# Kernel tuning notes

Measured on AMD Instinct MI355X. Metric: run time of the kernel, lower is better.

Reference implementation:

```python
import jax, jax.numpy as jnp
import numpy as np

INPUT_DIM = 128
OUTPUT_DIM = 256
BATCH = 4096

def setup_inputs() -> dict:
    key = jax.random.key(0)
    k_x, k_w1, k_b1, k_w2, k_b2 = jax.random.split(key, 5)
    d = INPUT_DIM
    h = 2 * OUTPUT_DIM
    x = jax.random.normal(k_x, (BATCH, d), dtype=jnp.float32)
    # Linear weights stored as [in, out]; scale ~ torch default init
    W1 = jax.random.uniform(k_w1, (d * d, h), dtype=jnp.float32, minval=-1, maxval=1) / np.sqrt(d * d)
    b1 = jax.random.uniform(k_b1, (h,), dtype=jnp.float32, minval=-1, maxval=1) / np.sqrt(d * d)
    W2 = jax.random.uniform(k_w2, (h, OUTPUT_DIM), dtype=jnp.float32, minval=-1, maxval=1) / np.sqrt(h)
    b2 = jax.random.uniform(k_b2, (OUTPUT_DIM,), dtype=jnp.float32, minval=-1, maxval=1) / np.sqrt(h)
    return {"x": x, "W1": W1, "b1": b1, "W2": W2, "b2": b2}

def reference(x, W1, b1, W2, b2):
    B, d = x.shape
    # torch bmm of the two expanded copies: tp[b,i,j] = sum_k x[b,i]*x[b,j] = d * x[b,i]*x[b,j]
    tp = jnp.asarray(d, x.dtype) * jnp.einsum('bi,bj->bij', x, x)  # [B, d, d]
    flat = tp.reshape(B, d * d)
    h = jax.nn.relu(flat @ W1 + b1)  # [B, 2*output_dim]
    return h @ W2 + b2               # [B, output_dim]
```

## Files before the change

kernel.cpp:

```cpp
#include <hip/hip_runtime.h>
#include <hip/hip_bf16.h>


typedef __attribute__((ext_vector_type(8))) short short8;
typedef __attribute__((ext_vector_type(4))) float floatx4;

__device__ __forceinline__ unsigned short f2bf(float f) {
    union { float f; unsigned int u; } v; v.f = f;
    unsigned int r = v.u + 0x7fffu + ((v.u >> 16) & 1u);
    return (unsigned short)(r >> 16);
}
__device__ __forceinline__ float bf2f(unsigned short b) {
    union { unsigned int u; float f; } v; v.u = ((unsigned int)b) << 16;
    return v.f;
}

__global__ __launch_bounds__(256) void pack_w1_kernel(
    const float* __restrict__ W1, unsigned short* __restrict__ W1Tp) {
    __shared__ float tile[64][65];
    const int k0 = blockIdx.x * 64;
    const int c0 = blockIdx.y * 64;
    const int tr = threadIdx.x >> 4;
    const int tc4 = (threadIdx.x & 15) * 4;
#pragma unroll
    for (int p = 0; p < 4; ++p) {
        int k = p * 16 + tr;
        float4 v = *(const float4*)(W1 + (long)(k0 + k) * 512 + c0 + tc4);
        tile[k][tc4 + 0] = v.x; tile[k][tc4 + 1] = v.y;
        tile[k][tc4 + 2] = v.z; tile[k][tc4 + 3] = v.w;
    }
    __syncthreads();
    const int lane = threadIdx.x & 63;
    const int w = threadIdx.x >> 6;
    const int m = lane & 15, quad = lane >> 4;
#pragma unroll
    for (int pass = 0; pass < 2; ++pass) {
        int chunk = w * 2 + pass;
        int kcL = chunk & 1, c16L = chunk >> 1;
        union { unsigned short s[8]; uint4 u; } o;
#pragma unroll
        for (int j = 0; j < 8; ++j)
            o.s[j] = f2bf(tile[kcL * 32 + quad * 8 + j][c16L * 16 + m]);
        long c16g = (c0 >> 4) + c16L;
        long kcg  = (k0 >> 5) + kcL;
        *(uint4*)(W1Tp + (c16g * 512 + kcg) * 512 + lane * 8) = o.u;
    }
}

__global__ __launch_bounds__(256) void transpose_cast_kernel(
    const float* __restrict__ in, unsigned short* __restrict__ out, int R, int C) {
    __shared__ float tile[64][65];
    const int r0 = blockIdx.x * 64, c0 = blockIdx.y * 64;
    const int tr = threadIdx.x >> 4;
    const int tc4 = (threadIdx.x & 15) * 4;
#pragma unroll
    for (int p = 0; p < 4; ++p) {
        int r = p * 16 + tr;
        float4 v = *(const float4*)(in + (long)(r0 + r) * C + c0 + tc4);
        tile[r][tc4 + 0] = v.x; tile[r][tc4 + 1] = v.y;
        tile[r][tc4 + 2] = v.z; tile[r][tc4 + 3] = v.w;
    }
    __syncthreads();
#pragma unroll
    for (int p = 0; p < 4; ++p) {
        int c = p * 16 + tr;
        union { unsigned short s[4]; uint2 u; } pk;
#pragma unroll
        for (int e = 0; e < 4; ++e) pk.s[e] = f2bf(tile[tc4 + e][c]);
        *(uint2*)(out + (long)(c0 + c) * R + r0 + tc4) = pk.u;
    }
}

__global__ __launch_bounds__(256, 2) void gemm1_kernel(
    const float* __restrict__ x,
    const unsigned short* __restrict__ W1Tp,
    unsigned short* __restrict__ Pb) {
    __shared__ float xT[256][34];
    const int tid = threadIdx.x;
    const int b0 = blockIdx.x * 256;
    const int c0 = blockIdx.y * 64;
    const int zi = blockIdx.z;
    const int i0 = zi * 32;

    for (int idx = tid; idx < 256 * 32; idx += 256) {
        int bL = idx >> 5, iL = idx & 31;
        xT[bL][iL] = x[(long)(b0 + bL) * 128 + i0 + iL];
    }
    __syncthreads();

    const int wid = tid >> 6;
    const int wm = wid >> 1, wn = wid & 1;
    const int lane = tid & 63;
    const int n16 = lane & 15, quad = lane >> 4;
    const int bBase = b0 + wn * 128;
    const int c16base = (c0 >> 4) + wm * 2;
    const int bLloc = wn * 128 + n16;

    floatx4 acc[2][8];
#pragma unroll
    for (int tm = 0; tm < 2; ++tm)
#pragma unroll
        for (int tn = 0; tn < 8; ++tn) acc[tm][tn] = (floatx4){0.f, 0.f, 0.f, 0.f};
    const floatx4 zero4 = (floatx4){0.f, 0.f, 0.f, 0.f};

#pragma unroll
    for (int jh = 0; jh < 2; ++jh) {
        short8 Xf[2][8];
#pragma unroll
        for (int ks = 0; ks < 2; ++ks)
#pragma unroll
            for (int tn = 0; tn < 8; ++tn) {
                const float* xp = x + (long)(bBase + tn * 16 + n16) * 128
                                    + jh * 64 + ks * 32 + quad * 8;
                float4 v0 = *(const float4*)xp;
                float4 v1 = *(const float4*)(xp + 4);
                short8 f;
                f[0] = (short)f2bf(v0.x); f[1] = (short)f2bf(v0.y);
                f[2] = (short)f2bf(v0.z); f[3] = (short)f2bf(v0.w);
                f[4] = (short)f2bf(v1.x); f[5] = (short)f2bf(v1.y);
                f[6] = (short)f2bf(v1.z); f[7] = (short)f2bf(v1.w);
                Xf[ks][tn] = f;
            }
        const unsigned short* aBase[2][2];
#pragma unroll
        for (int tm = 0; tm < 2; ++tm)
#pragma unroll
            for (int ks = 0; ks < 2; ++ks)
                aBase[tm][ks] = W1Tp
                    + ((long)(c16base + tm) * 512 + (long)i0 * 4 + jh * 2 + ks) * 512
                    + lane * 8;

        short8 Abuf[2][2][2];
#pragma unroll
        for (int tm = 0; tm < 2; ++tm)
#pragma unroll
            for (int ks = 0; ks < 2; ++ks) {
                Abuf[0][tm][ks] = *(const short8*)(aBase[tm][ks]);
                Abuf[1][tm][ks] = *(const short8*)(aBase[tm][ks] + 2048);
            }

#pragma unroll 2
        for (int i = 0; i < 32; ++i) {
            const int st = i & 1;
            float xi[8];
#pragma unroll
            for (int tn = 0; tn < 8; ++tn)
                xi[tn] = xT[bLloc + tn * 16][i];
#pragma unroll
            for (int tm = 0; tm < 2; ++tm)
#pragma unroll
                for (int tn = 0; tn < 8; ++tn) {
                    floatx4 t = __builtin_amdgcn_mfma_f32_16x16x32_bf16(
                        Abuf[st][tm][0], Xf[0][tn], zero4, 0, 0, 0);
                    t = __builtin_amdgcn_mfma_f32_16x16x32_bf16(
                        Abuf[st][tm][1], Xf[1][tn], t, 0, 0, 0);
                    acc[tm][tn] += xi[tn] * t;
                }
            const int pi = (i + 2) & 31;
#pragma unroll
            for (int tm = 0; tm < 2; ++tm)
#pragma unroll
                for (int ks = 0; ks < 2; ++ks)
                    Abuf[st][tm][ks] =
                        *(const short8*)(aBase[tm][ks] + (long)pi * 2048);
        }
    }

    unsigned short* pb = Pb + (long)zi * (4096L * 512);
#pragma unroll
    for (int tm = 0; tm < 2; ++tm)
#pragma unroll
        for (int tn = 0; tn < 8; ++tn) {
            int b = bBase + tn * 16 + n16;
            int cb = (c16base + tm) * 16 + quad * 4;
            union { unsigned short s[4]; uint2 u; } pk;
#pragma unroll
            for (int r = 0; r < 4; ++r) pk.s[r] = f2bf(acc[tm][tn][r]);
            *(uint2*)(pb + (long)b * 512 + cb) = pk.u;
        }
}

__global__ __launch_bounds__(256) void tail_kernel(
    const unsigned short* __restrict__ Pb,
    const float* __restrict__ b1,
    const unsigned short* __restrict__ W2T,
    const float* __restrict__ b2,
    float* __restrict__ out) {
    __shared__ unsigned short hL[16][516];
    __shared__ float b1s[512];
    const int tid = threadIdx.x;
    const int b0 = blockIdx.x * 16;
    b1s[tid] = b1[tid];
    b1s[tid + 256] = b1[tid + 256];
    __syncthreads();

    const unsigned int* Pu = (const unsigned int*)Pb;
#pragma unroll 4
    for (int idx = tid; idx < 16 * 256; idx += 256) {
        int bL = idx >> 8;
        int cu = idx & 255;
        float s0 = 0.f, s1 = 0.f;
#pragma unroll
        for (int z = 0; z < 4; ++z) {
            unsigned int u = Pu[((long)z * 4096 + b0 + bL) * 256 + cu];
            s0 += bf2f((unsigned short)(u & 0xffff));
            s1 += bf2f((unsigned short)(u >> 16));
        }
        int c = cu * 2;
        float v0 = fmaxf(fmaf(128.f, s0, b1s[c]), 0.f);
        float v1 = fmaxf(fmaf(128.f, s1, b1s[c + 1]), 0.f);
        unsigned int pk = (unsigned int)f2bf(v0) | ((unsigned int)f2bf(v1) << 16);
        *(unsigned int*)&hL[bL][c] = pk;
    }
    __syncthreads();

    const int w = tid >> 6, lane = tid & 63;
    const int n16 = lane & 15, quad = lane >> 4;
    const int o0 = w * 64;
    floatx4 acc[4];
#pragma unroll
    for (int tn = 0; tn < 4; ++tn) acc[tn] = (floatx4){0.f, 0.f, 0.f, 0.f};

#pragma unroll 4
    for (int ks = 0; ks < 16; ++ks) {
        short8 Af, Bf[4];
        {
            const unsigned short* p = &hL[n16][ks * 32 + quad * 8];
            union { uint2 u[2]; short8 s; } cvt;
            cvt.u[0] = *(const uint2*)p;
            cvt.u[1] = *(const uint2*)(p + 4);
            Af = cvt.s;
        }
#pragma unroll
        for (int tn = 0; tn < 4; ++tn)
            Bf[tn] = *(const short8*)(W2T + (long)(o0 + tn * 16 + n16) * 512
                                      + ks * 32 + quad * 8);
#pragma unroll
        for (int tn = 0; tn < 4; ++tn)
            acc[tn] = __builtin_amdgcn_mfma_f32_16x16x32_bf16(
                Af, Bf[tn], acc[tn], 0, 0, 0);
    }
#pragma unroll
    for (int tn = 0; tn < 4; ++tn) {
        float bias = b2[o0 + tn * 16 + n16];
#pragma unroll
        for (int r = 0; r < 4; ++r)
            out[(long)(b0 + quad * 4 + r) * 256
                + o0 + tn * 16 + n16] = acc[tn][r] + bias;
    }
}

extern "C" void kernel_launch(void* const* d_in, const int* in_sizes, int n_in,
                              void* d_out, int out_size, void* d_ws, size_t ws_size,
                              hipStream_t stream) {
    const float* x  = (const float*)d_in[0];
    const float* W1 = (const float*)d_in[1];
    const float* b1 = (const float*)d_in[2];
    const float* W2 = (const float*)d_in[3];
    const float* b2 = (const float*)d_in[4];
    float* out = (float*)d_out;

    char* ws = (char*)d_ws;
    unsigned short* W1Tp = (unsigned short*)(ws);
    unsigned short* W2T  = (unsigned short*)(ws + 16777216);
    unsigned short* Pb   = (unsigned short*)(ws + 16777216 + 262144);

    pack_w1_kernel<<<dim3(256, 8), 256, 0, stream>>>(W1, W1Tp);
    transpose_cast_kernel<<<dim3(8, 4), 256, 0, stream>>>(W2, W2T, 512, 256);
    gemm1_kernel<<<dim3(16, 8, 4), 256, 0, stream>>>(x, W1Tp, Pb);
    tail_kernel<<<dim3(256), 256, 0, stream>>>(Pb, b1, W2T, b2, out);
}
```

Baseline: 175.0 us.

## Shrink gemm1 block tile to 128 batch rows and one column tile per warp

Each gemm1 block now covers 128 batch rows instead of 256, and each warp owns a single 16-column strip of W1 instead of two. The grid doubles in x, which halves accumulator registers and shared memory per block and should allow more concurrent waves and better CU fill. The A-fragment double buffering is rewritten as an explicit two-stage manually unrolled loop with named registers in place of an indexed array. In exchange, each W1 fragment is reused across fewer batch rows, so global/L2 traffic for W1 roughly doubles.

New measurement: 184.7 us. +5.6%, slower.

```diff
diff --git a/kernel.cpp b/kernel.cpp
--- a/kernel.cpp
+++ b/kernel.cpp
@@ -75,32 +75,27 @@
     const float* __restrict__ x,
     const unsigned short* __restrict__ W1Tp,
     unsigned short* __restrict__ Pb) {
-    __shared__ float xT[256][34];
+    __shared__ float xT[128][33];
     const int tid = threadIdx.x;
-    const int b0 = blockIdx.x * 256;
+    const int b0 = blockIdx.x * 128;
     const int c0 = blockIdx.y * 64;
     const int zi = blockIdx.z;
     const int i0 = zi * 32;
 
-    for (int idx = tid; idx < 256 * 32; idx += 256) {
+    for (int idx = tid; idx < 128 * 32; idx += 256) {
         int bL = idx >> 5, iL = idx & 31;
         xT[bL][iL] = x[(long)(b0 + bL) * 128 + i0 + iL];
     }
     __syncthreads();
 
     const int wid = tid >> 6;
-    const int wm = wid >> 1, wn = wid & 1;
     const int lane = tid & 63;
     const int n16 = lane & 15, quad = lane >> 4;
-    const int bBase = b0 + wn * 128;
-    const int c16base = (c0 >> 4) + wm * 2;
-    const int bLloc = wn * 128 + n16;
-
-    floatx4 acc[2][8];
-#pragma unroll
-    for (int tm = 0; tm < 2; ++tm)
-#pragma unroll
-        for (int tn = 0; tn < 8; ++tn) acc[tm][tn] = (floatx4){0.f, 0.f, 0.f, 0.f};
+    const int c16 = (c0 >> 4) + wid;
+
+    floatx4 acc[8];
+#pragma unroll
+    for (int tn = 0; tn < 8; ++tn) acc[tn] = (floatx4){0.f, 0.f, 0.f, 0.f};
     const floatx4 zero4 = (floatx4){0.f, 0.f, 0.f, 0.f};
 
 #pragma unroll
@@ -110,7 +105,7 @@
         for (int ks = 0; ks < 2; ++ks)
 #pragma unroll
             for (int tn = 0; tn < 8; ++tn) {
-                const float* xp = x + (long)(bBase + tn * 16 + n16) * 128
+                const float* xp = x + (long)(b0 + tn * 16 + n16) * 128
                                     + jh * 64 + ks * 32 + quad * 8;
                 float4 v0 = *(const float4*)xp;
                 float4 v1 = *(const float4*)(xp + 4);
@@ -121,63 +116,65 @@
                 f[6] = (short)f2bf(v1.z); f[7] = (short)f2bf(v1.w);
                 Xf[ks][tn] = f;
             }
-        const unsigned short* aBase[2][2];
-#pragma unroll
-        for (int tm = 0; tm < 2; ++tm)
-#pragma unroll
-            for (int ks = 0; ks < 2; ++ks)
-                aBase[tm][ks] = W1Tp
-                    + ((long)(c16base + tm) * 512 + (long)i0 * 4 + jh * 2 + ks) * 512
-                    + lane * 8;
-
-        short8 Abuf[2][2][2];
-#pragma unroll
-        for (int tm = 0; tm < 2; ++tm)
-#pragma unroll
-            for (int ks = 0; ks < 2; ++ks) {
-                Abuf[0][tm][ks] = *(const short8*)(aBase[tm][ks]);
-                Abuf[1][tm][ks] = *(const short8*)(aBase[tm][ks] + 2048);
-            }
-
-#pragma unroll 2
-        for (int i = 0; i < 32; ++i) {
-            const int st = i & 1;
-            float xi[8];
-#pragma unroll
-            for (int tn = 0; tn < 8; ++tn)
-                xi[tn] = xT[bLloc + tn * 16][i];
-#pragma unroll
-            for (int tm = 0; tm < 2; ++tm)
+        const unsigned short* aB0 = W1Tp
+            + ((long)c16 * 512 + (long)i0 * 4 + jh * 2) * 512 + lane * 8;
+        const unsigned short* aB1 = aB0 + 512;
+
+        short8 A00 = *(const short8*)(aB0);
+        short8 A01 = *(const short8*)(aB1);
+        short8 A10 = *(const short8*)(aB0 + 2048);
+        short8 A11 = *(const short8*)(aB1 + 2048);
+
+#pragma unroll 1
+        for (int ib = 0; ib < 16; ++ib) {
+            const int i = ib * 2;
+            {
+                float xi[8];
+#pragma unroll
+                for (int tn = 0; tn < 8; ++tn)
+                    xi[tn] = xT[n16 + tn * 16][i];
 #pragma unroll
                 for (int tn = 0; tn < 8; ++tn) {
                     floatx4 t = __builtin_amdgcn_mfma_f32_16x16x32_bf16(
-                        Abuf[st][tm][0], Xf[0][tn], zero4, 0, 0, 0);
+                        A00, Xf[0][tn], zero4, 0, 0, 0);
                     t = __builtin_amdgcn_mfma_f32_16x16x32_bf16(
-                        Abuf[st][tm][1], Xf[1][tn], t, 0, 0, 0);
-                    acc[tm][tn] += xi[tn] * t;
+                        A01, Xf[1][tn], t, 0, 0, 0);
+                    acc[tn] += xi[tn] * t;
                 }
-            const int pi = (i + 2) & 31;
-#pragma unroll
-            for (int tm = 0; tm < 2; ++tm)
-#pragma unroll
-                for (int ks = 0; ks < 2; ++ks)
-                    Abuf[st][tm][ks] =
-                        *(const short8*)(aBase[tm][ks] + (long)pi * 2048);
+                const int p = (i + 2) & 31;
+                A00 = *(const short8*)(aB0 + (long)p * 2048);
+                A01 = *(const short8*)(aB1 + (long)p * 2048);
+            }
+            {
+                float xi[8];
+#pragma unroll
+                for (int tn = 0; tn < 8; ++tn)
+                    xi[tn] = xT[n16 + tn * 16][i + 1];
+#pragma unroll
+                for (int tn = 0; tn < 8; ++tn) {
+                    floatx4 t = __builtin_amdgcn_mfma_f32_16x16x32_bf16(
+                        A10, Xf[0][tn], zero4, 0, 0, 0);
+                    t = __builtin_amdgcn_mfma_f32_16x16x32_bf16(
+                        A11, Xf[1][tn], t, 0, 0, 0);
+                    acc[tn] += xi[tn] * t;
+                }
+                const int p = (i + 3) & 31;
+                A10 = *(const short8*)(aB0 + (long)p * 2048);
+                A11 = *(const short8*)(aB1 + (long)p * 2048);
+            }
         }
     }
 
     unsigned short* pb = Pb + (long)zi * (4096L * 512);
 #pragma unroll
-    for (int tm = 0; tm < 2; ++tm)
-#pragma unroll
-        for (int tn = 0; tn < 8; ++tn) {
-            int b = bBase + tn * 16 + n16;
-            int cb = (c16base + tm) * 16 + quad * 4;
-            union { unsigned short s[4]; uint2 u; } pk;
-#pragma unroll
-            for (int r = 0; r < 4; ++r) pk.s[r] = f2bf(acc[tm][tn][r]);
-            *(uint2*)(pb + (long)b * 512 + cb) = pk.u;
-        }
+    for (int tn = 0; tn < 8; ++tn) {
+        int b = b0 + tn * 16 + n16;
+        int cb = c16 * 16 + quad * 4;
+        union { unsigned short s[4]; uint2 u; } pk;
+#pragma unroll
+        for (int r = 0; r < 4; ++r) pk.s[r] = f2bf(acc[tn][r]);
+        *(uint2*)(pb + (long)b * 512 + cb) = pk.u;
+    }
 }
 
 __global__ __launch_bounds__(256) void tail_kernel(
@@ -267,6 +264,6 @@
 
     pack_w1_kernel<<<dim3(256, 8), 256, 0, stream>>>(W1, W1Tp);
     transpose_cast_kernel<<<dim3(8, 4), 256, 0, stream>>>(W2, W2T, 512, 256);
-    gemm1_kernel<<<dim3(16, 8, 4), 256, 0, stream>>>(x, W1Tp, Pb);
+    gemm1_kernel<<<dim3(32, 8, 4), 256, 0, stream>>>(x, W1Tp, Pb);
     tail_kernel<<<dim3(256), 256, 0, stream>>>(Pb, b1, W2T, b2, out);
 }
```

## Deepen W1 register prefetch to four stages and swizzle gemm1 block order

Applied to the files above, without the earlier changes.

The inner loop of gemm1 now keeps four stages of W1 fragments in named registers instead of a two-stage array, prefetching four iterations ahead through a macro-unrolled step. This is meant to hide global-load latency behind more MFMA work and to avoid dynamic array indexing. The 3D grid is flattened to 1D and remapped so that consecutive blocks are spread across different batch, column and z tiles, which changes how blocks are distributed over XCDs and how cache locality falls out. Extra prefetch registers can raise register pressure under the two-blocks-per-CU launch bound.

New measurement: 175.7 us. No clear change (+0.4%).

```diff
diff --git a/kernel.cpp b/kernel.cpp
--- a/kernel.cpp
+++ b/kernel.cpp
@@ -71,15 +71,44 @@
     }
 }
 
+
+#define A_STEP(Ac00, Ac01, Ac10, Ac11, I)                                  \
+    {                                                                      \
+        float xi[8];                                                       \
+        _Pragma("unroll")                                                  \
+        for (int tn = 0; tn < 8; ++tn)                                     \
+            xi[tn] = xT[bLloc + tn * 16][(I)];                             \
+        _Pragma("unroll")                                                  \
+        for (int tn = 0; tn < 8; ++tn) {                                   \
+            floatx4 t0 = __builtin_amdgcn_mfma_f32_16x16x32_bf16(          \
+                Ac00, Xf[0][tn], zero4, 0, 0, 0);                          \
+            t0 = __builtin_amdgcn_mfma_f32_16x16x32_bf16(                  \
+                Ac01, Xf[1][tn], t0, 0, 0, 0);                             \
+            acc[0][tn] += xi[tn] * t0;                                     \
+            floatx4 t1 = __builtin_amdgcn_mfma_f32_16x16x32_bf16(          \
+                Ac10, Xf[0][tn], zero4, 0, 0, 0);                          \
+            t1 = __builtin_amdgcn_mfma_f32_16x16x32_bf16(                  \
+                Ac11, Xf[1][tn], t1, 0, 0, 0);                             \
+            acc[1][tn] += xi[tn] * t1;                                     \
+        }                                                                  \
+        const int p_ = ((I) + 4) & 31;     \
+        Ac00 = *(const short8*)(aB00 + (long)p_ * 2048);                   \
+        Ac01 = *(const short8*)(aB01 + (long)p_ * 2048);                   \
+        Ac10 = *(const short8*)(aB10 + (long)p_ * 2048);                   \
+        Ac11 = *(const short8*)(aB11 + (long)p_ * 2048);                   \
+    }
+
 __global__ __launch_bounds__(256, 2) void gemm1_kernel(
     const float* __restrict__ x,
     const unsigned short* __restrict__ W1Tp,
     unsigned short* __restrict__ Pb) {
     __shared__ float xT[256][34];
     const int tid = threadIdx.x;
-    const int b0 = blockIdx.x * 256;
-    const int c0 = blockIdx.y * 64;
-    const int zi = blockIdx.z;
+    const int n = blockIdx.x;
+    const int L = (n & 7) * 64 + (n >> 3);
+    const int b0 = (L & 15) * 256;
+    const int c0 = ((L >> 4) & 7) * 64;
+    const int zi = L >> 7;
     const int i0 = zi * 32;
 
     for (int idx = tid; idx < 256 * 32; idx += 256) {
@@ -121,48 +150,39 @@
                 f[6] = (short)f2bf(v1.z); f[7] = (short)f2bf(v1.w);
                 Xf[ks][tn] = f;
             }
-        const unsigned short* aBase[2][2];
-#pragma unroll
-        for (int tm = 0; tm < 2; ++tm)
-#pragma unroll
-            for (int ks = 0; ks < 2; ++ks)
-                aBase[tm][ks] = W1Tp
-                    + ((long)(c16base + tm) * 512 + (long)i0 * 4 + jh * 2 + ks) * 512
-                    + lane * 8;
-
-        short8 Abuf[2][2][2];
-#pragma unroll
-        for (int tm = 0; tm < 2; ++tm)
-#pragma unroll
-            for (int ks = 0; ks < 2; ++ks) {
-                Abuf[0][tm][ks] = *(const short8*)(aBase[tm][ks]);
-                Abuf[1][tm][ks] = *(const short8*)(aBase[tm][ks] + 2048);
-            }
-
-#pragma unroll 2
-        for (int i = 0; i < 32; ++i) {
-            const int st = i & 1;
-            float xi[8];
-#pragma unroll
-            for (int tn = 0; tn < 8; ++tn)
-                xi[tn] = xT[bLloc + tn * 16][i];
-#pragma unroll
-            for (int tm = 0; tm < 2; ++tm)
-#pragma unroll
-                for (int tn = 0; tn < 8; ++tn) {
-                    floatx4 t = __builtin_amdgcn_mfma_f32_16x16x32_bf16(
-                        Abuf[st][tm][0], Xf[0][tn], zero4, 0, 0, 0);
-                    t = __builtin_amdgcn_mfma_f32_16x16x32_bf16(
-                        Abuf[st][tm][1], Xf[1][tn], t, 0, 0, 0);
-                    acc[tm][tn] += xi[tn] * t;
-                }
-            const int pi = (i + 2) & 31;
-#pragma unroll
-            for (int tm = 0; tm < 2; ++tm)
-#pragma unroll
-                for (int ks = 0; ks < 2; ++ks)
-                    Abuf[st][tm][ks] =
-                        *(const short8*)(aBase[tm][ks] + (long)pi * 2048);
+        const unsigned short* aB00 = W1Tp
+            + ((long)(c16base + 0) * 512 + (long)i0 * 4 + jh * 2 + 0) * 512
+            + lane * 8;
+        const unsigned short* aB01 = aB00 + 512;
+        const unsigned short* aB10 = W1Tp
+            + ((long)(c16base + 1) * 512 + (long)i0 * 4 + jh * 2 + 0) * 512
+            + lane * 8;
+        const unsigned short* aB11 = aB10 + 512;
+
+        short8 A0_00 = *(const short8*)(aB00);
+        short8 A0_01 = *(const short8*)(aB01);
+        short8 A0_10 = *(const short8*)(aB10);
+        short8 A0_11 = *(const short8*)(aB11);
+        short8 A1_00 = *(const short8*)(aB00 + 1 * 2048);
+        short8 A1_01 = *(const short8*)(aB01 + 1 * 2048);
+        short8 A1_10 = *(const short8*)(aB10 + 1 * 2048);
+        short8 A1_11 = *(const short8*)(aB11 + 1 * 2048);
+        short8 A2_00 = *(const short8*)(aB00 + 2 * 2048);
+        short8 A2_01 = *(const short8*)(aB01 + 2 * 2048);
+        short8 A2_10 = *(const short8*)(aB10 + 2 * 2048);
+        short8 A2_11 = *(const short8*)(aB11 + 2 * 2048);
+        short8 A3_00 = *(const short8*)(aB00 + 3 * 2048);
+        short8 A3_01 = *(const short8*)(aB01 + 3 * 2048);
+        short8 A3_10 = *(const short8*)(aB10 + 3 * 2048);
+        short8 A3_11 = *(const short8*)(aB11 + 3 * 2048);
+
+#pragma unroll 1
+        for (int ib = 0; ib < 8; ++ib) {
+            const int i = ib * 4;
+            A_STEP(A0_00, A0_01, A0_10, A0_11, i + 0)
+            A_STEP(A1_00, A1_01, A1_10, A1_11, i + 1)
+            A_STEP(A2_00, A2_01, A2_10, A2_11, i + 2)
+            A_STEP(A3_00, A3_01, A3_10, A3_11, i + 3)
         }
     }
 
@@ -267,6 +287,6 @@
 
     pack_w1_kernel<<<dim3(256, 8), 256, 0, stream>>>(W1, W1Tp);
     transpose_cast_kernel<<<dim3(8, 4), 256, 0, stream>>>(W2, W2T, 512, 256);
-    gemm1_kernel<<<dim3(16, 8, 4), 256, 0, stream>>>(x, W1Tp, Pb);
+    gemm1_kernel<<<dim3(512), 256, 0, stream>>>(x, W1Tp, Pb);
     tail_kernel<<<dim3(256), 256, 0, stream>>>(Pb, b1, W2T, b2, out);
 }
```

## Exploit outer-product symmetry to fold W1 into upper-triangular packed weights

Applied to the files above, without the earlier changes.

Because x_i*x_j is symmetric, the prep kernel folds W1[i,j]+W1[j,i] into an upper-triangular packed bf16 weight, so the first GEMM reads about 10 of 16 K-blocks. The first GEMM now covers the full K range per block instead of splitting over four z partitions. This removes the bf16 partial-sum buffer and the reduction pass, and bias plus ReLU move into the GEMM epilogue. The two prep kernels are merged into one launch, and the block-index mappings are swizzled. Folding the weight pairs before rounding to bf16 changes rounding slightly, and each GEMM block now has fewer output tiles and loops over more K.

After: 186.2 us. +6.4%, slower.

```diff
diff --git a/kernel.cpp b/kernel.cpp
--- a/kernel.cpp
+++ b/kernel.cpp
@@ -10,81 +10,130 @@
     unsigned int r = v.u + 0x7fffu + ((v.u >> 16) & 1u);
     return (unsigned short)(r >> 16);
 }
-__device__ __forceinline__ float bf2f(unsigned short b) {
-    union { unsigned int u; float f; } v; v.u = ((unsigned int)b) << 16;
-    return v.f;
-}
-
-__global__ __launch_bounds__(256) void pack_w1_kernel(
-    const float* __restrict__ W1, unsigned short* __restrict__ W1Tp) {
+
+__global__ __launch_bounds__(256) void prep_kernel(
+    const float* __restrict__ W1, unsigned short* __restrict__ W1p,
+    const float* __restrict__ W2, unsigned short* __restrict__ W2T) {
     __shared__ float tile[64][65];
-    const int k0 = blockIdx.x * 64;
-    const int c0 = blockIdx.y * 64;
-    const int tr = threadIdx.x >> 4;
-    const int tc4 = (threadIdx.x & 15) * 4;
-#pragma unroll
-    for (int p = 0; p < 4; ++p) {
-        int k = p * 16 + tr;
-        float4 v = *(const float4*)(W1 + (long)(k0 + k) * 512 + c0 + tc4);
-        tile[k][tc4 + 0] = v.x; tile[k][tc4 + 1] = v.y;
-        tile[k][tc4 + 2] = v.z; tile[k][tc4 + 3] = v.w;
-    }
-    __syncthreads();
-    const int lane = threadIdx.x & 63;
-    const int w = threadIdx.x >> 6;
-    const int m = lane & 15, quad = lane >> 4;
-#pragma unroll
-    for (int pass = 0; pass < 2; ++pass) {
-        int chunk = w * 2 + pass;
-        int kcL = chunk & 1, c16L = chunk >> 1;
-        union { unsigned short s[8]; uint4 u; } o;
-#pragma unroll
-        for (int j = 0; j < 8; ++j)
-            o.s[j] = f2bf(tile[kcL * 32 + quad * 8 + j][c16L * 16 + m]);
-        long c16g = (c0 >> 4) + c16L;
-        long kcg  = (k0 >> 5) + kcL;
-        *(uint4*)(W1Tp + (c16g * 512 + kcg) * 512 + lane * 8) = o.u;
-    }
-}
-
-__global__ __launch_bounds__(256) void transpose_cast_kernel(
-    const float* __restrict__ in, unsigned short* __restrict__ out, int R, int C) {
-    __shared__ float tile[64][65];
-    const int r0 = blockIdx.x * 64, c0 = blockIdx.y * 64;
-    const int tr = threadIdx.x >> 4;
-    const int tc4 = (threadIdx.x & 15) * 4;
-#pragma unroll
-    for (int p = 0; p < 4; ++p) {
-        int r = p * 16 + tr;
-        float4 v = *(const float4*)(in + (long)(r0 + r) * C + c0 + tc4);
-        tile[r][tc4 + 0] = v.x; tile[r][tc4 + 1] = v.y;
-        tile[r][tc4 + 2] = v.z; tile[r][tc4 + 3] = v.w;
-    }
-    __syncthreads();
-#pragma unroll
-    for (int p = 0; p < 4; ++p) {
-        int c = p * 16 + tr;
-        union { unsigned short s[4]; uint2 u; } pk;
-#pragma unroll
-        for (int e = 0; e < 4; ++e) pk.s[e] = f2bf(tile[tc4 + e][c]);
-        *(uint2*)(out + (long)(c0 + c) * R + r0 + tc4) = pk.u;
-    }
-}
-
-__global__ __launch_bounds__(256, 2) void gemm1_kernel(
+    const int bx = blockIdx.x;
+    if (bx < 320) {
+        const int cb = bx & 7;
+        const int ih = (bx >> 3) & 3;
+        const int p  = bx >> 5;
+        int zi, zj;
+        if (p < 4)      { zi = 0; zj = p; }
+        else if (p < 7) { zi = 1; zj = p - 3; }
+        else if (p < 9) { zi = 2; zj = p - 5; }
+        else            { zi = 3; zj = 3; }
+        const int lane = threadIdx.x & 63;
+        const int w = threadIdx.x >> 6;
+        const int m = lane & 15, quad = lane >> 4;
+        const int c16 = cb * 4 + w;
+        const int c = c16 * 16 + m;
+        const int cum = (zi == 0) ? 0 : (zi == 1) ? 128 : (zi == 2) ? 224 : 288;
+        for (int il8 = 0; il8 < 8; ++il8) {
+            const int il = ih * 8 + il8;
+            const int i_g = zi * 32 + il;
+            union { unsigned short s[8]; uint4 u; } o;
+#pragma unroll
+            for (int e = 0; e < 8; ++e) {
+                const int j_g = zj * 32 + quad * 8 + e;
+                float v = 0.f;
+                if (j_g == i_g)
+                    v = W1[((long)i_g * 128 + j_g) * 512 + c];
+                else if (j_g > i_g)
+                    v = W1[((long)i_g * 128 + j_g) * 512 + c]
+                      + W1[((long)j_g * 128 + i_g) * 512 + c];
+                o.s[e] = f2bf(v);
+            }
+            const long chunk = (long)c16 * 320 + cum
+                             + (long)il * (4 - zi) + (zj - zi);
+            *(uint4*)(W1p + chunk * 512 + lane * 8) = o.u;
+        }
+    } else {
+        const int t = bx - 320;
+        const int r0 = (t & 7) * 64, c0 = (t >> 3) * 64;
+        const int R = 512, C = 256;
+        const int tr = threadIdx.x >> 4;
+        const int tc4 = (threadIdx.x & 15) * 4;
+#pragma unroll
+        for (int pp = 0; pp < 4; ++pp) {
+            int r = pp * 16 + tr;
+            float4 v = *(const float4*)(W2 + (long)(r0 + r) * C + c0 + tc4);
+            tile[r][tc4 + 0] = v.x; tile[r][tc4 + 1] = v.y;
+            tile[r][tc4 + 2] = v.z; tile[r][tc4 + 3] = v.w;
+        }
+        __syncthreads();
+#pragma unroll
+        for (int pp = 0; pp < 4; ++pp) {
+            int cc = pp * 16 + tr;
+            union { unsigned short s[4]; uint2 u; } pk;
+#pragma unroll
+            for (int e = 0; e < 4; ++e) pk.s[e] = f2bf(tile[tc4 + e][cc]);
+            *(uint2*)(W2T + (long)(c0 + cc) * R + r0 + tc4) = pk.u;
+        }
+    }
+}
+
+
+#define Z_PHASE(CH, ZB)                                                     \
+    {                                                                       \
+        short8 Ar[2][2][CH];                                                \
+        _Pragma("unroll")                                                   \
+        for (int q = 0; q < CH; ++q) {                                      \
+            Ar[0][0][q] = *(const short8*)(aP0 + (long)q * 512);            \
+            Ar[0][1][q] = *(const short8*)(aP1 + (long)q * 512);            \
+            Ar[1][0][q] = *(const short8*)(aP0 + (long)(CH + q) * 512);     \
+            Ar[1][1][q] = *(const short8*)(aP1 + (long)(CH + q) * 512);     \
+        }                                                                   \
+        _Pragma("unroll 2")                                                 \
+        for (int il = 0; il < 32; ++il) {                                   \
+            const int st = il & 1;                                          \
+            float xi0 = xT[xrow0][(ZB) * 32 + il];                          \
+            float xi1 = xT[xrow1][(ZB) * 32 + il];                          \
+            floatx4 t00 = zero4, t01 = zero4, t10 = zero4, t11 = zero4;     \
+            _Pragma("unroll")                                               \
+            for (int q = 0; q < CH; ++q) {                                  \
+                t00 = __builtin_amdgcn_mfma_f32_16x16x32_bf16(              \
+                    Ar[st][0][q], Xf[4 - (CH) + q][0], t00, 0, 0, 0);       \
+                t01 = __builtin_amdgcn_mfma_f32_16x16x32_bf16(              \
+                    Ar[st][0][q], Xf[4 - (CH) + q][1], t01, 0, 0, 0);       \
+                t10 = __builtin_amdgcn_mfma_f32_16x16x32_bf16(              \
+                    Ar[st][1][q], Xf[4 - (CH) + q][0], t10, 0, 0, 0);       \
+                t11 = __builtin_amdgcn_mfma_f32_16x16x32_bf16(              \
+                    Ar[st][1][q], Xf[4 - (CH) + q][1], t11, 0, 0, 0);       \
+            }                                                               \
+            acc[0][0] += xi0 * t00; acc[0][1] += xi1 * t01;                 \
+            acc[1][0] += xi0 * t10; acc[1][1] += xi1 * t11;                 \
+            _Pragma("unroll")                                               \
+            for (int q = 0; q < CH; ++q) {                                  \
+                Ar[st][0][q] = *(const short8*)(aP0                         \
+                    + (long)((il + 2) * (CH) + q) * 512);                   \
+                Ar[st][1][q] = *(const short8*)(aP1                         \
+                    + (long)((il + 2) * (CH) + q) * 512);                   \
+            }                                                               \
+        }                                                                   \
+        aP0 += 32 * (CH) * 512;                                             \
+        aP1 += 32 * (CH) * 512;                                             \
+    }
+
+__global__ __launch_bounds__(256, 2) void gemm_sym_kernel(
     const float* __restrict__ x,
-    const unsigned short* __restrict__ W1Tp,
-    unsigned short* __restrict__ Pb) {
-    __shared__ float xT[256][34];
+    const unsigned short* __restrict__ W1p,
+    const float* __restrict__ b1,
+    unsigned short* __restrict__ H) {
+    __shared__ float xT[64][129];
     const int tid = threadIdx.x;
-    const int b0 = blockIdx.x * 256;
-    const int c0 = blockIdx.y * 64;
-    const int zi = blockIdx.z;
-    const int i0 = zi * 32;
-
-    for (int idx = tid; idx < 256 * 32; idx += 256) {
-        int bL = idx >> 5, iL = idx & 31;
-        xT[bL][iL] = x[(long)(b0 + bL) * 128 + i0 + iL];
+    const int n = blockIdx.x;
+    const int L = (n & 7) * 64 + (n >> 3);
+    const int b0 = (L & 63) * 64;
+    const int c0 = (L >> 6) * 64;
+
+    for (int idx = tid; idx < 64 * 32; idx += 256) {
+        int bL = idx >> 5, i4 = (idx & 31) * 4;
+        float4 v = *(const float4*)(x + (long)(b0 + bL) * 128 + i4);
+        xT[bL][i4 + 0] = v.x; xT[bL][i4 + 1] = v.y;
+        xT[bL][i4 + 2] = v.z; xT[bL][i4 + 3] = v.w;
     }
     __syncthreads();
 
@@ -92,128 +141,70 @@
     const int wm = wid >> 1, wn = wid & 1;
     const int lane = tid & 63;
     const int n16 = lane & 15, quad = lane >> 4;
-    const int bBase = b0 + wn * 128;
+    const int bBase = b0 + wn * 32;
     const int c16base = (c0 >> 4) + wm * 2;
-    const int bLloc = wn * 128 + n16;
-
-    floatx4 acc[2][8];
+    const int xrow0 = wn * 32 + n16;
+    const int xrow1 = xrow0 + 16;
+
+    floatx4 acc[2][2];
 #pragma unroll
     for (int tm = 0; tm < 2; ++tm)
 #pragma unroll
-        for (int tn = 0; tn < 8; ++tn) acc[tm][tn] = (floatx4){0.f, 0.f, 0.f, 0.f};
+        for (int tn = 0; tn < 2; ++tn) acc[tm][tn] = (floatx4){0.f, 0.f, 0.f, 0.f};
     const floatx4 zero4 = (floatx4){0.f, 0.f, 0.f, 0.f};
 
-#pragma unroll
-    for (int jh = 0; jh < 2; ++jh) {
-        short8 Xf[2][8];
-#pragma unroll
-        for (int ks = 0; ks < 2; ++ks)
-#pragma unroll
-            for (int tn = 0; tn < 8; ++tn) {
-                const float* xp = x + (long)(bBase + tn * 16 + n16) * 128
-                                    + jh * 64 + ks * 32 + quad * 8;
-                float4 v0 = *(const float4*)xp;
-                float4 v1 = *(const float4*)(xp + 4);
-                short8 f;
-                f[0] = (short)f2bf(v0.x); f[1] = (short)f2bf(v0.y);
-                f[2] = (short)f2bf(v0.z); f[3] = (short)f2bf(v0.w);
-                f[4] = (short)f2bf(v1.x); f[5] = (short)f2bf(v1.y);
-                f[6] = (short)f2bf(v1.z); f[7] = (short)f2bf(v1.w);
-                Xf[ks][tn] = f;
-            }
-        const unsigned short* aBase[2][2];
-#pragma unroll
-        for (int tm = 0; tm < 2; ++tm)
-#pragma unroll
-            for (int ks = 0; ks < 2; ++ks)
-                aBase[tm][ks] = W1Tp
-                    + ((long)(c16base + tm) * 512 + (long)i0 * 4 + jh * 2 + ks) * 512
-                    + lane * 8;
-
-        short8 Abuf[2][2][2];
-#pragma unroll
-        for (int tm = 0; tm < 2; ++tm)
-#pragma unroll
-            for (int ks = 0; ks < 2; ++ks) {
-                Abuf[0][tm][ks] = *(const short8*)(aBase[tm][ks]);
-                Abuf[1][tm][ks] = *(const short8*)(aBase[tm][ks] + 2048);
-            }
-
-#pragma unroll 2
-        for (int i = 0; i < 32; ++i) {
-            const int st = i & 1;
-            float xi[8];
-#pragma unroll
-            for (int tn = 0; tn < 8; ++tn)
-                xi[tn] = xT[bLloc + tn * 16][i];
-#pragma unroll
-            for (int tm = 0; tm < 2; ++tm)
-#pragma unroll
-                for (int tn = 0; tn < 8; ++tn) {
-                    floatx4 t = __builtin_amdgcn_mfma_f32_16x16x32_bf16(
-                        Abuf[st][tm][0], Xf[0][tn], zero4, 0, 0, 0);
-                    t = __builtin_amdgcn_mfma_f32_16x16x32_bf16(
-                        Abuf[st][tm][1], Xf[1][tn], t, 0, 0, 0);
-                    acc[tm][tn] += xi[tn] * t;
-                }
-            const int pi = (i + 2) & 31;
-#pragma unroll
-            for (int tm = 0; tm < 2; ++tm)
-#pragma unroll
-                for (int ks = 0; ks < 2; ++ks)
-                    Abuf[st][tm][ks] =
-                        *(const short8*)(aBase[tm][ks] + (long)pi * 2048);
-        }
-    }
-
-    unsigned short* pb = Pb + (long)zi * (4096L * 512);
-#pragma unroll
-    for (int tm = 0; tm < 2; ++tm)
-#pragma unroll
-        for (int tn = 0; tn < 8; ++tn) {
+    short8 Xf[4][2];
+#pragma unroll
+    for (int kc = 0; kc < 4; ++kc)
+#pragma unroll
+        for (int tn = 0; tn < 2; ++tn) {
+            const float* xp = x + (long)(bBase + tn * 16 + n16) * 128
+                                + kc * 32 + quad * 8;
+            float4 v0 = *(const float4*)xp;
+            float4 v1 = *(const float4*)(xp + 4);
+            short8 f;
+            f[0] = (short)f2bf(v0.x); f[1] = (short)f2bf(v0.y);
+            f[2] = (short)f2bf(v0.z); f[3] = (short)f2bf(v0.w);
+            f[4] = (short)f2bf(v1.x); f[5] = (short)f2bf(v1.y);
+            f[6] = (short)f2bf(v1.z); f[7] = (short)f2bf(v1.w);
+            Xf[kc][tn] = f;
+        }
+
+    const unsigned short* aP0 = W1p + (long)(c16base + 0) * 320 * 512 + lane * 8;
+    const unsigned short* aP1 = W1p + (long)(c16base + 1) * 320 * 512 + lane * 8;
+
+    Z_PHASE(4, 0)
+    Z_PHASE(3, 1)
+    Z_PHASE(2, 2)
+    Z_PHASE(1, 3)
+
+#pragma unroll
+    for (int tm = 0; tm < 2; ++tm) {
+        const int cb4 = (c16base + tm) * 16 + quad * 4;
+        float4 b1v = *(const float4*)(b1 + cb4);
+#pragma unroll
+        for (int tn = 0; tn < 2; ++tn) {
             int b = bBase + tn * 16 + n16;
-            int cb = (c16base + tm) * 16 + quad * 4;
             union { unsigned short s[4]; uint2 u; } pk;
-#pragma unroll
-            for (int r = 0; r < 4; ++r) pk.s[r] = f2bf(acc[tm][tn][r]);
-            *(uint2*)(pb + (long)b * 512 + cb) = pk.u;
-        }
+            pk.s[0] = f2bf(fmaxf(fmaf(128.f, acc[tm][tn][0], b1v.x), 0.f));
+            pk.s[1] = f2bf(fmaxf(fmaf(128.f, acc[tm][tn][1], b1v.y), 0.f));
+            pk.s[2] = f2bf(fmaxf(fmaf(128.f, acc[tm][tn][2], b1v.z), 0.f));
+            pk.s[3] = f2bf(fmaxf(fmaf(128.f, acc[tm][tn][3], b1v.w), 0.f));
+            *(uint2*)(H + (long)b * 512 + cb4) = pk.u;
+        }
+    }
 }
 
 __global__ __launch_bounds__(256) void tail_kernel(
-    const unsigned short* __restrict__ Pb,
-    const float* __restrict__ b1,
+    const unsigned short* __restrict__ H,
     const unsigned short* __restrict__ W2T,
     const float* __restrict__ b2,
     float* __restrict__ out) {
-    __shared__ unsigned short hL[16][516];
-    __shared__ float b1s[512];
     const int tid = threadIdx.x;
-    const int b0 = blockIdx.x * 16;
-    b1s[tid] = b1[tid];
-    b1s[tid + 256] = b1[tid + 256];
-    __syncthreads();
-
-    const unsigned int* Pu = (const unsigned int*)Pb;
-#pragma unroll 4
-    for (int idx = tid; idx < 16 * 256; idx += 256) {
-        int bL = idx >> 8;
-        int cu = idx & 255;
-        float s0 = 0.f, s1 = 0.f;
-#pragma unroll
-        for (int z = 0; z < 4; ++z) {
-            unsigned int u = Pu[((long)z * 4096 + b0 + bL) * 256 + cu];
-            s0 += bf2f((unsigned short)(u & 0xffff));
-            s1 += bf2f((unsigned short)(u >> 16));
-        }
-        int c = cu * 2;
-        float v0 = fmaxf(fmaf(128.f, s0, b1s[c]), 0.f);
-        float v1 = fmaxf(fmaf(128.f, s1, b1s[c + 1]), 0.f);
-        unsigned int pk = (unsigned int)f2bf(v0) | ((unsigned int)f2bf(v1) << 16);
-        *(unsigned int*)&hL[bL][c] = pk;
-    }
-    __syncthreads();
-
+    const int n = blockIdx.x;
+    const int v = n >> 3;
+    const int bt = (n & 7) * 4 + (v & 3) + (v >> 2) * 32;
+    const int b0 = bt * 16;
     const int w = tid >> 6, lane = tid & 63;
     const int n16 = lane & 15, quad = lane >> 4;
     const int o0 = w * 64;
@@ -223,14 +214,9 @@
 
 #pragma unroll 4
     for (int ks = 0; ks < 16; ++ks) {
-        short8 Af, Bf[4];
-        {
-            const unsigned short* p = &hL[n16][ks * 32 + quad * 8];
-            union { uint2 u[2]; short8 s; } cvt;
-            cvt.u[0] = *(const uint2*)p;
-            cvt.u[1] = *(const uint2*)(p + 4);
-            Af = cvt.s;
-        }
+        short8 Af = *(const short8*)(H + (long)(b0 + n16) * 512
+                                     + ks * 32 + quad * 8);
+        short8 Bf[4];
 #pragma unroll
         for (int tn = 0; tn < 4; ++tn)
             Bf[tn] = *(const short8*)(W2T + (long)(o0 + tn * 16 + n16) * 512
@@ -261,12 +247,11 @@
     float* out = (float*)d_out;
 
     char* ws = (char*)d_ws;
-    unsigned short* W1Tp = (unsigned short*)(ws);
-    unsigned short* W2T  = (unsigned short*)(ws + 16777216);
-    unsigned short* Pb   = (unsigned short*)(ws + 16777216 + 262144);
-
-    pack_w1_kernel<<<dim3(256, 8), 256, 0, stream>>>(W1, W1Tp);
-    transpose_cast_kernel<<<dim3(8, 4), 256, 0, stream>>>(W2, W2T, 512, 256);
-    gemm1_kernel<<<dim3(16, 8, 4), 256, 0, stream>>>(x, W1Tp, Pb);
-    tail_kernel<<<dim3(256), 256, 0, stream>>>(Pb, b1, W2T, b2, out);
-}
+    unsigned short* W1p = (unsigned short*)(ws);
+    unsigned short* W2T = (unsigned short*)(ws + 10485760);
+    unsigned short* H   = (unsigned short*)(ws + 10485760 + 262144);
+
+    prep_kernel<<<dim3(352), 256, 0, stream>>>(W1, W1p, W2, W2T);
+    gemm_sym_kernel<<<dim3(512), 256, 0, stream>>>(x, W1p, b1, H);
+    tail_kernel<<<dim3(256), 256, 0, stream>>>(H, W2T, b2, out);
+}
```
